# Kernel tuning notes

Hardware: AMD Instinct MI355X
Metric: run time of the kernel (lower is better)

The kernel has to match this reference:

```python
import jax, jax.numpy as jnp
import numpy as np

N = 50000      # nodes
E = 800000     # edges
P = 100000     # pos/neg candidate edges
IN = 128       # input feat dim
H, D = 2, 64   # heads, out_feats per head
HD = H * D     # 128
NEG_SLOPE = 0.2


def setup_inputs() -> dict:
    key = jax.random.key(0)
    ks = jax.random.split(key, 18)
    def gn(k, shape, fan_in):
        return jax.random.normal(k, shape, jnp.float32) * (1.0 / np.sqrt(fan_in))
    return {
        "x": jax.random.normal(ks[0], (N, IN), jnp.float32),
        "src": jax.random.randint(ks[1], (E,), 0, N),
        "dst": jax.random.randint(ks[2], (E,), 0, N),
        "pos_src": jax.random.randint(ks[3], (P,), 0, N),
        "pos_dst": jax.random.randint(ks[4], (P,), 0, N),
        "neg_src": jax.random.randint(ks[5], (P,), 0, N),
        "neg_dst": jax.random.randint(ks[6], (P,), 0, N),
        "W0": gn(ks[7], (IN, HD), IN),
        "attn0": gn(ks[8], (H, D), D),
        "W1": gn(ks[9], (HD, HD), HD),
        "attn1": gn(ks[10], (H, D), D),
        "Wp1": gn(ks[11], (HD, D), HD),
        "bp1": jnp.zeros((D,), jnp.float32),
        "Wp2": gn(ks[12], (D, D), D),
        "bp2": jnp.zeros((D,), jnp.float32),
        "Wp3": gn(ks[13], (D, 1), D),
        "bp3": jnp.zeros((1,), jnp.float32),
    }


def gatv2_layer(h, W, attn, src, dst, residual):
    # DGL GATv2Conv, share_weights=True, bias=False, feat_drop=attn_drop=0
    feat = (h @ W).reshape(N, H, D)            # [N,H,D]
    el = feat[src]                              # [E,H,D] gather at src
    er = feat[dst]                              # [E,H,D] gather at dst
    e = jax.nn.leaky_relu(el + er, NEG_SLOPE)   # [E,H,D]
    score = jnp.einsum('ehd,hd->eh', e, attn)   # [E,H]
    # edge softmax over incoming edges of each dst node
    m = jax.ops.segment_max(score, dst, num_segments=N)      # [N,H]
    p = jnp.exp(score - m[dst])                               # [E,H]
    s = jax.ops.segment_sum(p, dst, num_segments=N)           # [N,H]
    a = p / s[dst]                                             # [E,H]
    rst = jax.ops.segment_sum(el * a[:, :, None], dst, num_segments=N)  # [N,H,D]
    if residual:
        rst = rst + h.reshape(N, H, D)          # identity res_fc (dims match)
    return jax.nn.elu(rst).reshape(N, HD)       # flatten(1)


def reference(x, src, dst, pos_src, pos_dst, neg_src, neg_dst,
              W0, attn0, W1, attn1, Wp1, bp1, Wp2, bp2, Wp3, bp3):
    h = gatv2_layer(x, W0, attn0, src, dst, residual=False)
    h = gatv2_layer(h, W1, attn1, src, dst, residual=True)

    def predictor(z):
        z = jax.nn.relu(z @ Wp1 + bp1)
        z = jax.nn.relu(z @ Wp2 + bp2)
        return z @ Wp3 + bp3

    h_pos = predictor(h[pos_src] * h[pos_dst])  # [P,1]
    h_neg = predictor(h[neg_src] * h[neg_dst])  # [P,1]
    return (h_pos, h_neg)
```

## Files before the change

### kernel.cpp

```cpp
#include <hip/hip_runtime.h>
#include <math.h>

#define NN 50000
#define NE 800000
#define NP 100000
#define NEG_SLOPE 0.2f


__global__ void count_deg(const int* __restrict__ dst, int* __restrict__ cnt) {
    int i = blockIdx.x * blockDim.x + threadIdx.x;
    int st = gridDim.x * blockDim.x;
    for (; i < NE; i += st) atomicAdd(&cnt[dst[i]], 1);
}

__global__ __launch_bounds__(1024) void scan_deg(const int* __restrict__ cnt,
                                                 int* __restrict__ rowptr,
                                                 int* __restrict__ cursor) {
    __shared__ int wsum[16];
    __shared__ int carry;
    __shared__ int total;
    int tid = threadIdx.x;
    int lane = tid & 63, w = tid >> 6;
    if (tid == 0) carry = 0;
    __syncthreads();
    for (int base = 0; base < NN; base += 1024) {
        int idx = base + tid;
        int v = (idx < NN) ? cnt[idx] : 0;
        int x = v;
        #pragma unroll
        for (int mm = 1; mm < 64; mm <<= 1) {
            int y = __shfl_up(x, mm, 64);
            if (lane >= mm) x += y;
        }
        if (lane == 63) wsum[w] = x;
        __syncthreads();
        if (w == 0) {
            int orig = (lane < 16) ? wsum[lane] : 0;
            int t = orig;
            #pragma unroll
            for (int mm = 1; mm < 16; mm <<= 1) {
                int y = __shfl_up(t, mm, 64);
                if (lane >= mm) t += y;
            }
            if (lane < 16) wsum[lane] = t - orig;
            if (lane == 15) total = t;
        }
        __syncthreads();
        int excl = carry + wsum[w] + x - v;
        if (idx < NN) { rowptr[idx] = excl; cursor[idx] = excl; }
        __syncthreads();
        if (tid == 0) carry += total;
        __syncthreads();
    }
    if (tid == 0) rowptr[NN] = carry;
}

__global__ void scatter_edges(const int* __restrict__ src, const int* __restrict__ dst,
                              int* __restrict__ cursor, int* __restrict__ csrc) {
    int i = blockIdx.x * blockDim.x + threadIdx.x;
    int st = gridDim.x * blockDim.x;
    for (; i < NE; i += st) {
        int p = atomicAdd(&cursor[dst[i]], 1);
        csrc[p] = src[i];
    }
}


__global__ __launch_bounds__(256) void gemm128(const float* __restrict__ A,
                                               const float* __restrict__ W,
                                               float* __restrict__ out, int nrows) {
    __shared__ float Wt[128 * 132];
    __shared__ float rb[16 * 132];
    int tid = threadIdx.x;
    for (int idx = tid; idx < 128 * 128; idx += 256) {
        int k = idx >> 7, j = idx & 127;
        Wt[j * 132 + k] = W[idx];
    }
    __syncthreads();
    int lane = tid & 63, w = tid >> 6;
    int ntiles = (nrows + 15) >> 4;
    const float* w0p = &Wt[lane * 132];
    const float* w1p = &Wt[(64 + lane) * 132];
    for (int t = blockIdx.x; t < ntiles; t += gridDim.x) {
        int r0 = t << 4;
        for (int i = tid; i < 512; i += 256) {
            int rr = r0 + (i >> 5);
            float4 v = {0.f, 0.f, 0.f, 0.f};
            if (rr < nrows) v = ((const float4*)A)[(size_t)rr * 32 + (i & 31)];
            *(float4*)&rb[(i >> 5) * 132 + (i & 31) * 4] = v;
        }
        __syncthreads();
        float acc[4][2] = {};
        #pragma unroll 4
        for (int k4 = 0; k4 < 32; ++k4) {
            float4 wv0 = *(const float4*)&w0p[k4 * 4];
            float4 wv1 = *(const float4*)&w1p[k4 * 4];
            #pragma unroll
            for (int i2 = 0; i2 < 4; ++i2) {
                float4 av = *(const float4*)&rb[(w * 4 + i2) * 132 + k4 * 4];
                acc[i2][0] = fmaf(av.x, wv0.x, acc[i2][0]);
                acc[i2][0] = fmaf(av.y, wv0.y, acc[i2][0]);
                acc[i2][0] = fmaf(av.z, wv0.z, acc[i2][0]);
                acc[i2][0] = fmaf(av.w, wv0.w, acc[i2][0]);
                acc[i2][1] = fmaf(av.x, wv1.x, acc[i2][1]);
                acc[i2][1] = fmaf(av.y, wv1.y, acc[i2][1]);
                acc[i2][1] = fmaf(av.z, wv1.z, acc[i2][1]);
                acc[i2][1] = fmaf(av.w, wv1.w, acc[i2][1]);
            }
        }
        #pragma unroll
        for (int i2 = 0; i2 < 4; ++i2) {
            int rr = r0 + w * 4 + i2;
            if (rr < nrows) {
                out[(size_t)rr * 128 + lane]      = acc[i2][0];
                out[(size_t)rr * 128 + 64 + lane] = acc[i2][1];
            }
        }
        __syncthreads();
    }
}


__global__ void gat_fused(const float* __restrict__ feat,
                          const int* __restrict__ rowptr,
                          const int* __restrict__ csrc,
                          const float* __restrict__ attn,
                          const float* __restrict__ resid,
                          float* __restrict__ out) {
    int lane = threadIdx.x & 63;
    int wid = (blockIdx.x * blockDim.x + threadIdx.x) >> 6;
    int nw = (gridDim.x * blockDim.x) >> 6;
    int half = lane >> 5;
    int q = lane & 31;
    const float4* feat4 = (const float4*)feat;
    float4 at = ((const float4*)attn)[q];
    for (int d = wid; d < NN; d += nw) {
        int beg = rowptr[d], end = rowptr[d + 1];
        float4 fd = feat4[(size_t)d * 32 + q];
        float m = -INFINITY, s = 0.f;
        float ax = 0.f, ay = 0.f, az = 0.f, aw = 0.f;
        bool first = true;
        int i = beg + half;
        int sn = (i < end) ? csrc[i] : 0;
        float4 f = {0.f, 0.f, 0.f, 0.f};
        if (i < end) f = feat4[(size_t)sn * 32 + q];
        int snn = (i + 2 < end) ? csrc[i + 2] : 0;
        while (i < end) {
            float4 fn = {0.f, 0.f, 0.f, 0.f};
            if (i + 2 < end) fn = feat4[(size_t)snn * 32 + q];
            int sn2 = (i + 4 < end) ? csrc[i + 4] : 0;
            float ex = f.x + fd.x; ex = ex > 0.f ? ex : NEG_SLOPE * ex;
            float ey = f.y + fd.y; ey = ey > 0.f ? ey : NEG_SLOPE * ey;
            float ez = f.z + fd.z; ez = ez > 0.f ? ez : NEG_SLOPE * ez;
            float ew = f.w + fd.w; ew = ew > 0.f ? ew : NEG_SLOPE * ew;
            float part = ex * at.x + ey * at.y + ez * at.z + ew * at.w;
            part += __shfl_xor(part, 8, 64);
            part += __shfl_xor(part, 4, 64);
            part += __shfl_xor(part, 2, 64);
            part += __shfl_xor(part, 1, 64);
            float p = first ? 1.f : __expf(part - m);
            m = first ? part : m;
            first = false;
            s += p;
            ax = fmaf(f.x, p, ax);
            ay = fmaf(f.y, p, ay);
            az = fmaf(f.z, p, az);
            aw = fmaf(f.w, p, aw);
            f = fn; snn = sn2; i += 2;
        }
        float mo = __shfl_xor(m, 32, 64);
        float so = __shfl_xor(s, 32, 64);
        float ox = __shfl_xor(ax, 32, 64);
        float oy = __shfl_xor(ay, 32, 64);
        float oz = __shfl_xor(az, 32, 64);
        float ow = __shfl_xor(aw, 32, 64);
        float nm = fmaxf(m, mo);
        float sc0 = (m == nm) ? 1.f : __expf(m - nm);
        float sc1 = (mo == nm) ? 1.f : __expf(mo - nm);
        float S = s * sc0 + so * sc1;
        float inv = S > 0.f ? 1.f / S : 0.f;
        float vx = (ax * sc0 + ox * sc1) * inv;
        float vy = (ay * sc0 + oy * sc1) * inv;
        float vz = (az * sc0 + oz * sc1) * inv;
        float vw = (aw * sc0 + ow * sc1) * inv;
        if (resid) {
            float4 r = ((const float4*)resid)[(size_t)d * 32 + q];
            vx += r.x; vy += r.y; vz += r.z; vw += r.w;
        }
        vx = vx > 0.f ? vx : expm1f(vx);
        vy = vy > 0.f ? vy : expm1f(vy);
        vz = vz > 0.f ? vz : expm1f(vz);
        vw = vw > 0.f ? vw : expm1f(vw);
        if (half == 0) {
            float4 o; o.x = vx; o.y = vy; o.z = vz; o.w = vw;
            ((float4*)out)[(size_t)d * 32 + q] = o;
        }
    }
}


__global__ __launch_bounds__(768, 1) void predictor(const float* __restrict__ h,
                          const int* __restrict__ ps, const int* __restrict__ pd,
                          const int* __restrict__ ns, const int* __restrict__ nd,
                          const float* __restrict__ Wp1, const float* __restrict__ bp1,
                          const float* __restrict__ Wp2, const float* __restrict__ bp2,
                          const float* __restrict__ Wp3, const float* __restrict__ bp3,
                          float* __restrict__ out) {
    __shared__ float S[38144];
    int tid = threadIdx.x;
    for (int idx = tid; idx < 128 * 64; idx += 768) {
        int k = idx >> 6, c = idx & 63;
        S[c * 132 + k] = Wp1[idx];
    }
    for (int idx = tid; idx < 64 * 64; idx += 768) {
        int k = idx >> 6, c = idx & 63;
        S[8448 + c * 68 + k] = Wp2[idx];
    }
    __syncthreads();
    int lane = tid & 63;
    int w = tid >> 6;
    int cg = lane & 15, rg = lane >> 4;
    float* zz = S + 12800 + w * 2112;
    float b1v[4], b2v[4], w3v[4];
    #pragma unroll
    for (int i = 0; i < 4; ++i) {
        b1v[i] = bp1[cg + 16 * i];
        b2v[i] = bp2[cg + 16 * i];
        w3v[i] = Wp3[cg + 16 * i];
    }
    float b3 = bp3[0];
    int gw = blockIdx.x * 12 + w;
    int gnw = gridDim.x * 12;
    int ge = lane >> 2, gp = lane & 3;
    const float4* h4 = (const float4*)h;
    const int NT = (2 * NP) / 16;
    for (int T = gw; T < NT; T += gnw) {
        int e = T * 16 + ge;
        int a, b;
        if (e < NP) { a = ps[e]; b = pd[e]; }
        else        { a = ns[e - NP]; b = nd[e - NP]; }
        const float4* pa = h4 + (size_t)a * 32 + gp;
        const float4* pb = h4 + (size_t)b * 32 + gp;
        #pragma unroll
        for (int qq = 0; qq < 8; ++qq) {
            float4 va = pa[qq * 4];
            float4 vb = pb[qq * 4];
            float4 vz;
            vz.x = va.x * vb.x; vz.y = va.y * vb.y;
            vz.z = va.z * vb.z; vz.w = va.w * vb.w;
            *(float4*)&zz[ge * 132 + gp * 4 + qq * 16] = vz;
        }
        float acc[4][4] = {};
        #pragma unroll 4
        for (int k4 = 0; k4 < 32; ++k4) {
            float4 wv[4], zv[4];
            #pragma unroll
            for (int i = 0; i < 4; ++i)
                wv[i] = *(const float4*)&S[(cg + 16 * i) * 132 + k4 * 4];
            #pragma unroll
            for (int j = 0; j < 4; ++j)
                zv[j] = *(const float4*)&zz[(rg * 4 + j) * 132 + k4 * 4];
            #pragma unroll
            for (int j = 0; j < 4; ++j) {
                #pragma unroll
                for (int i = 0; i < 4; ++i) {
                    acc[j][i] = fmaf(zv[j].x, wv[i].x, acc[j][i]);
                    acc[j][i] = fmaf(zv[j].y, wv[i].y, acc[j][i]);
                    acc[j][i] = fmaf(zv[j].z, wv[i].z, acc[j][i]);
                    acc[j][i] = fmaf(zv[j].w, wv[i].w, acc[j][i]);
                }
            }
        }
        #pragma unroll
        for (int j = 0; j < 4; ++j) {
            #pragma unroll
            for (int i = 0; i < 4; ++i)
                zz[(rg * 4 + j) * 68 + cg + 16 * i] = fmaxf(acc[j][i] + b1v[i], 0.f);
        }
        float acc2[4][4] = {};
        #pragma unroll 4
        for (int k4 = 0; k4 < 16; ++k4) {
            float4 wv[4], zv[4];
            #pragma unroll
            for (int i = 0; i < 4; ++i)
                wv[i] = *(const float4*)&S[8448 + (cg + 16 * i) * 68 + k4 * 4];
            #pragma unroll
            for (int j = 0; j < 4; ++j)
                zv[j] = *(const float4*)&zz[(rg * 4 + j) * 68 + k4 * 4];
            #pragma unroll
            for (int j = 0; j < 4; ++j) {
                #pragma unroll
                for (int i = 0; i < 4; ++i) {
                    acc2[j][i] = fmaf(zv[j].x, wv[i].x, acc2[j][i]);
                    acc2[j][i] = fmaf(zv[j].y, wv[i].y, acc2[j][i]);
                    acc2[j][i] = fmaf(zv[j].z, wv[i].z, acc2[j][i]);
                    acc2[j][i] = fmaf(zv[j].w, wv[i].w, acc2[j][i]);
                }
            }
        }
        float v[4];
        #pragma unroll
        for (int j = 0; j < 4; ++j) {
            float sv = 0.f;
            #pragma unroll
            for (int i = 0; i < 4; ++i)
                sv = fmaf(fmaxf(acc2[j][i] + b2v[i], 0.f), w3v[i], sv);
            v[j] = sv;
        }
        #pragma unroll
        for (int mm = 1; mm <= 8; mm <<= 1) {
            #pragma unroll
            for (int j = 0; j < 4; ++j) v[j] += __shfl_xor(v[j], mm, 64);
        }
        if (cg == 0) {
            float4 o;
            o.x = v[0] + b3; o.y = v[1] + b3; o.z = v[2] + b3; o.w = v[3] + b3;
            *(float4*)&out[T * 16 + rg * 4] = o;
        }
    }
}

extern "C" void kernel_launch(void* const* d_in, const int* in_sizes, int n_in,
                              void* d_out, int out_size, void* d_ws, size_t ws_size,
                              hipStream_t stream) {
    const float* x       = (const float*)d_in[0];
    const int*   src     = (const int*)d_in[1];
    const int*   dst     = (const int*)d_in[2];
    const int*   pos_src = (const int*)d_in[3];
    const int*   pos_dst = (const int*)d_in[4];
    const int*   neg_src = (const int*)d_in[5];
    const int*   neg_dst = (const int*)d_in[6];
    const float* W0      = (const float*)d_in[7];
    const float* attn0   = (const float*)d_in[8];
    const float* W1      = (const float*)d_in[9];
    const float* attn1   = (const float*)d_in[10];
    const float* Wp1     = (const float*)d_in[11];
    const float* bp1     = (const float*)d_in[12];
    const float* Wp2     = (const float*)d_in[13];
    const float* bp2     = (const float*)d_in[14];
    const float* Wp3     = (const float*)d_in[15];
    const float* bp3     = (const float*)d_in[16];

    float* A = (float*)d_ws;
    float* B = A + (size_t)NN * 128;
    float* C = B + (size_t)NN * 128;
    int* cnt    = (int*)(C + (size_t)NN * 128);
    int* rowptr = cnt + NN;
    int* cursor = rowptr + NN + 1;
    int* csrc   = cursor + NN;
    float* out = (float*)d_out;

    hipMemsetAsync(cnt, 0, NN * sizeof(int), stream);
    count_deg<<<3125, 256, 0, stream>>>(dst, cnt);
    scan_deg<<<1, 1024, 0, stream>>>(cnt, rowptr, cursor);
    scatter_edges<<<3125, 256, 0, stream>>>(src, dst, cursor, csrc);

    gemm128<<<1024, 256, 0, stream>>>(x, W0, A, NN);
    gat_fused<<<3125, 256, 0, stream>>>(A, rowptr, csrc, attn0, nullptr, C);

    gemm128<<<1024, 256, 0, stream>>>(C, W1, A, NN);
    gat_fused<<<3125, 256, 0, stream>>>(A, rowptr, csrc, attn1, C, B);

    predictor<<<256, 768, 0, stream>>>(B, pos_src, pos_dst, neg_src, neg_dst,
                                       Wp1, bp1, Wp2, bp2, Wp3, bp3, out);
}
```

Before: 451.5 us.

## Assign one half-wave per node in GAT aggregation, use DPP row reductions

The GAT aggregation kernel now gives each 32-lane half-wave its own destination node instead of splitting one node's edges across two halves. That removes the cross-half softmax merge and doubles the number of nodes processed at once, and it uses a three-deep prefetch of neighbour features. The 16-lane score reduction in both GAT and the predictor is replaced with DPP row operations instead of shuffles. The predictor block shrinks from 12 to 8 waves with a smaller shared buffer, which trades per-block parallelism for possibly higher occupancy.

Result: faster. 440.3 us (-2.5%).

```diff
diff --git a/kernel.cpp b/kernel.cpp
--- a/kernel.cpp
+++ b/kernel.cpp
@@ -5,6 +5,18 @@
 #define NE 800000
 #define NP 100000
 #define NEG_SLOPE 0.2f
+
+__device__ __forceinline__ float row_sum16(float v) {
+    int x = __float_as_int(v);
+    v += __int_as_float(__builtin_amdgcn_update_dpp(0, x, 0x128, 0xF, 0xF, true));
+    x = __float_as_int(v);
+    v += __int_as_float(__builtin_amdgcn_update_dpp(0, x, 0x124, 0xF, 0xF, true));
+    x = __float_as_int(v);
+    v += __int_as_float(__builtin_amdgcn_update_dpp(0, x, 0x4E, 0xF, 0xF, true));
+    x = __float_as_int(v);
+    v += __int_as_float(__builtin_amdgcn_update_dpp(0, x, 0xB1, 0xF, 0xF, true));
+    return v;
+}
 
 
 __global__ void count_deg(const int* __restrict__ dst, int* __restrict__ cnt) {
@@ -127,62 +139,49 @@
                           const float* __restrict__ attn,
                           const float* __restrict__ resid,
                           float* __restrict__ out) {
-    int lane = threadIdx.x & 63;
-    int wid = (blockIdx.x * blockDim.x + threadIdx.x) >> 6;
-    int nw = (gridDim.x * blockDim.x) >> 6;
-    int half = lane >> 5;
-    int q = lane & 31;
+    int tid = blockIdx.x * blockDim.x + threadIdx.x;
+    int hw = tid >> 5;
+    int nhw = (gridDim.x * blockDim.x) >> 5;
+    int q = threadIdx.x & 31;
     const float4* feat4 = (const float4*)feat;
     float4 at = ((const float4*)attn)[q];
-    for (int d = wid; d < NN; d += nw) {
+    for (int d = hw; d < NN; d += nhw) {
         int beg = rowptr[d], end = rowptr[d + 1];
         float4 fd = feat4[(size_t)d * 32 + q];
-        float m = -INFINITY, s = 0.f;
+        float m = 0.f, s = 0.f;
         float ax = 0.f, ay = 0.f, az = 0.f, aw = 0.f;
         bool first = true;
-        int i = beg + half;
-        int sn = (i < end) ? csrc[i] : 0;
-        float4 f = {0.f, 0.f, 0.f, 0.f};
-        if (i < end) f = feat4[(size_t)sn * 32 + q];
-        int snn = (i + 2 < end) ? csrc[i + 2] : 0;
+        int i = beg;
+        float4 f0 = {0.f,0.f,0.f,0.f}, f1 = {0.f,0.f,0.f,0.f}, f2 = {0.f,0.f,0.f,0.f};
+        if (i     < end) f0 = feat4[(size_t)csrc[i]     * 32 + q];
+        if (i + 1 < end) f1 = feat4[(size_t)csrc[i + 1] * 32 + q];
+        if (i + 2 < end) f2 = feat4[(size_t)csrc[i + 2] * 32 + q];
+        int s3 = (i + 3 < end) ? csrc[i + 3] : 0;
         while (i < end) {
-            float4 fn = {0.f, 0.f, 0.f, 0.f};
-            if (i + 2 < end) fn = feat4[(size_t)snn * 32 + q];
-            int sn2 = (i + 4 < end) ? csrc[i + 4] : 0;
-            float ex = f.x + fd.x; ex = ex > 0.f ? ex : NEG_SLOPE * ex;
-            float ey = f.y + fd.y; ey = ey > 0.f ? ey : NEG_SLOPE * ey;
-            float ez = f.z + fd.z; ez = ez > 0.f ? ez : NEG_SLOPE * ez;
-            float ew = f.w + fd.w; ew = ew > 0.f ? ew : NEG_SLOPE * ew;
+            float4 f3 = {0.f, 0.f, 0.f, 0.f};
+            if (i + 3 < end) f3 = feat4[(size_t)s3 * 32 + q];
+            int s4 = (i + 4 < end) ? csrc[i + 4] : 0;
+            float ex = f0.x + fd.x; ex = ex > 0.f ? ex : NEG_SLOPE * ex;
+            float ey = f0.y + fd.y; ey = ey > 0.f ? ey : NEG_SLOPE * ey;
+            float ez = f0.z + fd.z; ez = ez > 0.f ? ez : NEG_SLOPE * ez;
+            float ew = f0.w + fd.w; ew = ew > 0.f ? ew : NEG_SLOPE * ew;
             float part = ex * at.x + ey * at.y + ez * at.z + ew * at.w;
-            part += __shfl_xor(part, 8, 64);
-            part += __shfl_xor(part, 4, 64);
-            part += __shfl_xor(part, 2, 64);
-            part += __shfl_xor(part, 1, 64);
+            part = row_sum16(part);
             float p = first ? 1.f : __expf(part - m);
             m = first ? part : m;
             first = false;
             s += p;
-            ax = fmaf(f.x, p, ax);
-            ay = fmaf(f.y, p, ay);
-            az = fmaf(f.z, p, az);
-            aw = fmaf(f.w, p, aw);
-            f = fn; snn = sn2; i += 2;
-        }
-        float mo = __shfl_xor(m, 32, 64);
-        float so = __shfl_xor(s, 32, 64);
-        float ox = __shfl_xor(ax, 32, 64);
-        float oy = __shfl_xor(ay, 32, 64);
-        float oz = __shfl_xor(az, 32, 64);
-        float ow = __shfl_xor(aw, 32, 64);
-        float nm = fmaxf(m, mo);
-        float sc0 = (m == nm) ? 1.f : __expf(m - nm);
-        float sc1 = (mo == nm) ? 1.f : __expf(mo - nm);
-        float S = s * sc0 + so * sc1;
-        float inv = S > 0.f ? 1.f / S : 0.f;
-        float vx = (ax * sc0 + ox * sc1) * inv;
-        float vy = (ay * sc0 + oy * sc1) * inv;
-        float vz = (az * sc0 + oz * sc1) * inv;
-        float vw = (aw * sc0 + ow * sc1) * inv;
+            ax = fmaf(f0.x, p, ax);
+            ay = fmaf(f0.y, p, ay);
+            az = fmaf(f0.z, p, az);
+            aw = fmaf(f0.w, p, aw);
+            f0 = f1; f1 = f2; f2 = f3; s3 = s4; ++i;
+        }
+        float inv = s > 0.f ? 1.f / s : 0.f;
+        float vx = ax * inv;
+        float vy = ay * inv;
+        float vz = az * inv;
+        float vw = aw * inv;
         if (resid) {
             float4 r = ((const float4*)resid)[(size_t)d * 32 + q];
             vx += r.x; vy += r.y; vz += r.z; vw += r.w;
@@ -191,28 +190,26 @@
         vy = vy > 0.f ? vy : expm1f(vy);
         vz = vz > 0.f ? vz : expm1f(vz);
         vw = vw > 0.f ? vw : expm1f(vw);
-        if (half == 0) {
-            float4 o; o.x = vx; o.y = vy; o.z = vz; o.w = vw;
-            ((float4*)out)[(size_t)d * 32 + q] = o;
-        }
-    }
-}
-
-
-__global__ __launch_bounds__(768, 1) void predictor(const float* __restrict__ h,
+        float4 o; o.x = vx; o.y = vy; o.z = vz; o.w = vw;
+        ((float4*)out)[(size_t)d * 32 + q] = o;
+    }
+}
+
+
+__global__ __launch_bounds__(512, 1) void predictor(const float* __restrict__ h,
                           const int* __restrict__ ps, const int* __restrict__ pd,
                           const int* __restrict__ ns, const int* __restrict__ nd,
                           const float* __restrict__ Wp1, const float* __restrict__ bp1,
                           const float* __restrict__ Wp2, const float* __restrict__ bp2,
                           const float* __restrict__ Wp3, const float* __restrict__ bp3,
                           float* __restrict__ out) {
-    __shared__ float S[38144];
+    __shared__ float S[29696];
     int tid = threadIdx.x;
-    for (int idx = tid; idx < 128 * 64; idx += 768) {
+    for (int idx = tid; idx < 128 * 64; idx += 512) {
         int k = idx >> 6, c = idx & 63;
         S[c * 132 + k] = Wp1[idx];
     }
-    for (int idx = tid; idx < 64 * 64; idx += 768) {
+    for (int idx = tid; idx < 64 * 64; idx += 512) {
         int k = idx >> 6, c = idx & 63;
         S[8448 + c * 68 + k] = Wp2[idx];
     }
@@ -229,8 +226,8 @@
         w3v[i] = Wp3[cg + 16 * i];
     }
     float b3 = bp3[0];
-    int gw = blockIdx.x * 12 + w;
-    int gnw = gridDim.x * 12;
+    int gw = blockIdx.x * 8 + w;
+    int gnw = gridDim.x * 8;
     int ge = lane >> 2, gp = lane & 3;
     const float4* h4 = (const float4*)h;
     const int NT = (2 * NP) / 16;
@@ -305,12 +302,7 @@
             #pragma unroll
             for (int i = 0; i < 4; ++i)
                 sv = fmaf(fmaxf(acc2[j][i] + b2v[i], 0.f), w3v[i], sv);
-            v[j] = sv;
-        }
-        #pragma unroll
-        for (int mm = 1; mm <= 8; mm <<= 1) {
-            #pragma unroll
-            for (int j = 0; j < 4; ++j) v[j] += __shfl_xor(v[j], mm, 64);
+            v[j] = row_sum16(sv);
         }
         if (cg == 0) {
             float4 o;
@@ -361,6 +353,6 @@
     gemm128<<<1024, 256, 0, stream>>>(C, W1, A, NN);
     gat_fused<<<3125, 256, 0, stream>>>(A, rowptr, csrc, attn1, C, B);
 
-    predictor<<<256, 768, 0, stream>>>(B, pos_src, pos_dst, neg_src, neg_dst,
+    predictor<<<256, 512, 0, stream>>>(B, pos_src, pos_dst, neg_src, neg_dst,
                                        Wp1, bp1, Wp2, bp2, Wp3, bp3, out);
 }
```
